# Optimization experiments

Hardware: AMD Instinct MI355X
Metric: run time of the kernel (lower is better)

Reference implementation:

```python
import jax, jax.numpy as jnp
import numpy as np

EPS = 1e-6      # vnn EPS used in norms / leaky-relu denominators
BN_EPS = 1e-5   # torch BatchNorm eps
K = 20          # args.n_knn


def vnlin(W, x):
    # VNLinear: apply (O,C) weight over channel axis 1 of x (B,C,3,...)
    return jnp.moveaxis(jnp.tensordot(W, x, axes=((1,), (1,))), 0, 1)


def vn_bn(x):
    # VNBatchNorm (training-mode batch stats, affine = identity init):
    # normalizes the per-vector norms, rescales vectors accordingly.
    norm = jnp.sqrt(jnp.sum(x * x, axis=2)) + EPS        # (B,C,...)
    axes = (0,) + tuple(range(2, norm.ndim))             # per-channel stats
    mean = jnp.mean(norm, axis=axes, keepdims=True)
    var = jnp.var(norm, axis=axes, keepdims=True)
    norm_bn = (norm - mean) / jnp.sqrt(var + BN_EPS)
    return x / jnp.expand_dims(norm, 2) * jnp.expand_dims(norm_bn, 2)


def vn_lrelu(Wf, Wd, x):
    # VNLinearLeakyReLU with negative_slope=0 (as constructed in this module)
    p = vn_bn(vnlin(Wf, x))
    d = vnlin(Wd, x)
    dot = jnp.sum(p * d, axis=2, keepdims=True)
    dsq = jnp.sum(d * d, axis=2, keepdims=True)
    return jnp.where(dot >= 0, p, p - (dot / (dsq + EPS)) * d)


def vn_maxpool(Wd, x):
    # VNMaxPool: pool over last axis, picking per (b,c) the vector maximizing <x,d>
    d = vnlin(Wd, x)
    dot = jnp.sum(x * d, axis=2, keepdims=True)          # (B,C,1,...)
    idx = jnp.argmax(dot, axis=-1)                       # (B,C,1,...)
    idx = jnp.broadcast_to(idx[..., None], x.shape[:-1] + (1,))
    return jnp.take_along_axis(x, idx, axis=-1)[..., 0]


def graph_feature_cross(x, k):
    # x: (B,3,N) -> (B, 3ch, 3vec, N, k); channels = [nbr-x, x, cross(nbr,x)]
    xx = jnp.sum(x * x, axis=1)                          # (B,N)
    inner = jnp.einsum('bdi,bdj->bij', x, x)             # (B,N,N)
    pd = 2.0 * inner - xx[:, :, None] - xx[:, None, :]   # = -||xi-xj||^2
    idx = jax.lax.top_k(pd, k)[1]                        # (B,N,k) nearest
    pts = jnp.swapaxes(x, 1, 2)                          # (B,N,3)
    nb = jax.vmap(lambda p, i: p[i])(pts, idx)           # (B,N,k,3) gather
    c = jnp.broadcast_to(pts[:, :, None, :], nb.shape)   # center repeated
    cross = jnp.cross(nb, c)
    feat = jnp.stack([nb - c, c, cross], axis=3)         # (B,N,k,3,3)
    return jnp.transpose(feat, (0, 3, 4, 1, 2))


_W_SPECS = {
    'pos_Wf': (21, 3), 'pos_Wd': (21, 3), 'pool_Wd': (21, 21),
    'c1_Wf': (21, 21), 'c1_Wd': (21, 21),
    'st1_Wf': (21, 21), 'st1_Wd': (21, 21),
    'st2_Wf': (42, 21), 'st2_Wd': (42, 21),
    'st3_Wf': (341, 42), 'st3_Wd': (341, 42),
    'st_pool_Wd': (341, 341),
    'stf1_Wf': (170, 341), 'stf1_Wd': (170, 341),
    'stf2_Wf': (85, 170), 'stf2_Wd': (85, 170),
    'stf3_W': (21, 85),
    'c2_Wf': (42, 42), 'c2_Wd': (42, 42),
    'c3_W': (341, 42),
    'std1_Wf': (341, 682), 'std1_Wd': (341, 682),
    'std2_Wf': (170, 341), 'std2_Wd': (170, 341),
    'std_lin': (3, 170),
}


def setup_inputs() -> dict:
    key = jax.random.key(0)
    ks = iter(jax.random.split(key, 32))
    inp = {'x': jax.random.normal(next(ks), (8, 3, 4096), dtype=jnp.float32)}
    for name, (o, i) in _W_SPECS.items():
        inp[name] = jax.random.normal(next(ks), (o, i), dtype=jnp.float32) / np.sqrt(i).astype(np.float32)
    return inp


def _forward(x, pos_Wf, pos_Wd, pool_Wd, c1_Wf, c1_Wd, st1_Wf, st1_Wd, st2_Wf, st2_Wd,
             st3_Wf, st3_Wd, st_pool_Wd, stf1_Wf, stf1_Wd, stf2_Wf, stf2_Wd, stf3_W,
             c2_Wf, c2_Wd, c3_W, std1_Wf, std1_Wd, std2_Wf, std2_Wd, std_lin):
    B, D, N = x.shape
    feat = graph_feature_cross(x, K)                     # (B,3,3,N,k)
    h = vn_lrelu(pos_Wf, pos_Wd, feat)                   # (B,21,3,N,k)
    h = vn_maxpool(pool_Wd, h)                           # (B,21,3,N) pool over k
    h = vn_lrelu(c1_Wf, c1_Wd, h)                        # (B,21,3,N)
    # STNkd feature transform
    s = vn_lrelu(st1_Wf, st1_Wd, h)                      # (B,21,3,N)
    s = vn_lrelu(st2_Wf, st2_Wd, s)                      # (B,42,3,N)
    s = vn_lrelu(st3_Wf, st3_Wd, s)                      # (B,341,3,N)
    s = vn_maxpool(st_pool_Wd, s)                        # (B,341,3) pool over N
    s = vn_lrelu(stf1_Wf, stf1_Wd, s)                    # (B,170,3)
    s = vn_lrelu(stf2_Wf, stf2_Wd, s)                    # (B,85,3)
    s = vnlin(stf3_W, s)                                 # (B,21,3)
    s = jnp.broadcast_to(s[..., None], h.shape)          # repeat over N
    h = jnp.concatenate([h, s], axis=1)                  # (B,42,3,N)
    h = vn_lrelu(c2_Wf, c2_Wd, h)                        # (B,42,3,N)
    h = vn_bn(vnlin(c3_W, h))                            # (B,341,3,N)
    h_mean = jnp.broadcast_to(jnp.mean(h, axis=-1, keepdims=True), h.shape)
    h = jnp.concatenate([h, h_mean], axis=1)             # (B,682,3,N)
    # VNStdFeature (normalize_frame=False)
    z0 = vn_lrelu(std1_Wf, std1_Wd, h)                   # (B,341,3,N)
    z0 = vn_lrelu(std2_Wf, std2_Wd, z0)                  # (B,170,3,N)
    z0 = vnlin(std_lin, z0)                              # (B,3,3,N)
    h_std = jnp.einsum('bijm,bjkm->bikm', h, z0)         # (B,682,3,N)
    out = jnp.max(h_std.reshape(B, -1, N), axis=-1)      # (B,2046)
    return out, z0


def reference(x, pos_Wf, pos_Wd, pool_Wd, c1_Wf, c1_Wd, st1_Wf, st1_Wd, st2_Wf, st2_Wd,
              st3_Wf, st3_Wd, st_pool_Wd, stf1_Wf, stf1_Wd, stf2_Wf, stf2_Wd, stf3_W,
              c2_Wf, c2_Wd, c3_W, std1_Wf, std1_Wd, std2_Wf, std2_Wd, std_lin):
    return _forward(x, pos_Wf, pos_Wd, pool_Wd, c1_Wf, c1_Wd, st1_Wf, st1_Wd, st2_Wf,
                    st2_Wd, st3_Wf, st3_Wd, st_pool_Wd, stf1_Wf, stf1_Wd, stf2_Wf,
                    stf2_Wd, stf3_W, c2_Wf, c2_Wd, c3_W, std1_Wf, std1_Wd, std2_Wf,
                    std2_Wd, std_lin)
```

## Files before the change

kernel.cpp:

```cpp
#include <hip/hip_runtime.h>
#include <cstdint>
#include <cstddef>


typedef unsigned short u16;
using bh8  = __attribute__((ext_vector_type(8))) short;
using f32x4 = __attribute__((ext_vector_type(4))) float;

__device__ __forceinline__ float b2f(u16 v) {
  return __uint_as_float(((unsigned)v) << 16);
}
__device__ __forceinline__ u16 f2b(float f) {
  unsigned u = __float_as_uint(f);
  u += 0x7FFFu + ((u >> 16) & 1u);
  return (u16)(u >> 16);
}

__device__ __forceinline__ float ldg(const float* p, size_t i) { return p[i]; }
__device__ __forceinline__ float ldg(const u16* p, size_t i) { return b2f(p[i]); }
__device__ __forceinline__ void st4(float* p, size_t i, float a, float b, float c, float d) {
  float4 v; v.x = a; v.y = b; v.z = c; v.w = d; *(float4*)(p + i) = v;
}

#define FMA4(A, S, V) { A.x += (S)*(V).x; A.y += (S)*(V).y; A.z += (S)*(V).z; A.w += (S)*(V).w; }

__device__ __forceinline__ unsigned long long packKey(float v, int n) {
  unsigned u = __float_as_uint(v);
  u = (u & 0x80000000u) ? ~u : (u | 0x80000000u);
  return ((unsigned long long)u << 32) | (unsigned long long)(0xFFFFFFFFu - (unsigned)n);
}

#define CSWAP(T) { if (c > T) { unsigned long long tmp = T; T = c; c = tmp; } }
__global__ __launch_bounds__(256) void knn_kernel(const float* __restrict__ x,
                                                  int* __restrict__ idxOut, int N) {
  int b = blockIdx.y;
  int wv = threadIdx.x >> 6, lane = threadIdx.x & 63;
  int i = blockIdx.x * 4 + wv;
  const float* xb = x + (size_t)b * 3 * N;
  float xi0 = xb[i], xi1 = xb[N + i], xi2 = xb[2 * (size_t)N + i];
  float xxi = xi0 * xi0 + xi1 * xi1 + xi2 * xi2;
  unsigned long long t0 = 0, t1 = 0, t2 = 0, t3 = 0, t4 = 0, t5 = 0, t6 = 0, t7 = 0;
  #pragma unroll 8
  for (int s = 0; s < 64; ++s) {
    int j = s * 64 + lane;
    float a0 = xb[j], a1 = xb[N + j], a2 = xb[2 * (size_t)N + j];
    float inner = xi0 * a0 + xi1 * a1 + xi2 * a2;
    float xxj = a0 * a0 + a1 * a1 + a2 * a2;
    float pd = 2.f * inner - xxi - xxj;
    unsigned long long c = packKey(pd, j);
    if (c > t7) { CSWAP(t0) CSWAP(t1) CSWAP(t2) CSWAP(t3) CSWAP(t4) CSWAP(t5) CSWAP(t6) CSWAP(t7) }
  }
  int* row = idxOut + ((size_t)b * N + i) * 20;
  for (int kk = 0; kk < 20; ++kk) {
    unsigned long long k = t0;
    #pragma unroll
    for (int off = 1; off < 64; off <<= 1) {
      unsigned long long o = __shfl_xor(k, off);
      if (o > k) k = o;
    }
    if (lane == 0) row[kk] = (int)(0xFFFFFFFFu - (unsigned)(k & 0xFFFFFFFFull));
    if (k == t0) { t0 = t1; t1 = t2; t2 = t3; t3 = t4; t4 = t5; t5 = t6; t6 = t7; t7 = 0; }
  }
}
#undef CSWAP

__global__ __launch_bounds__(256) void pos_stats(const float* __restrict__ x,
                                                 const int* __restrict__ idx,
                                                 const float* __restrict__ Wf,
                                                 float* __restrict__ statSum,
                                                 float* __restrict__ statSq, int N) {
  __shared__ float wf[64];
  __shared__ float part[4][42];
  int tid = threadIdx.x;
  if (tid < 63) wf[tid] = Wf[tid];
  __syncthreads();
  int b = blockIdx.y;
  int lin = blockIdx.x * 256 + tid;
  int n = lin / 20, kk = lin - n * 20;
  const float* xb = x + (size_t)b * 3 * N;
  int j = idx[((size_t)b * N + n) * 20 + kk];
  float c0 = xb[n], c1 = xb[N + n], c2 = xb[2 * (size_t)N + n];
  float a0 = xb[j], a1 = xb[N + j], a2 = xb[2 * (size_t)N + j];
  float e00 = a0 - c0, e01 = a1 - c1, e02 = a2 - c2;
  float e20 = a1 * c2 - a2 * c1, e21 = a2 * c0 - a0 * c2, e22 = a0 * c1 - a1 * c0;
  int lane = tid & 63, wave = tid >> 6;
  #pragma unroll
  for (int c = 0; c < 21; ++c) {
    float w0 = wf[c * 3], w1 = wf[c * 3 + 1], w2 = wf[c * 3 + 2];
    float p0 = w0 * e00 + w1 * c0 + w2 * e20;
    float p1 = w0 * e01 + w1 * c1 + w2 * e21;
    float p2 = w0 * e02 + w1 * c2 + w2 * e22;
    float nr = sqrtf(p0 * p0 + p1 * p1 + p2 * p2) + 1e-6f;
    float u1 = nr, u2 = nr * nr;
    #pragma unroll
    for (int off = 32; off; off >>= 1) { u1 += __shfl_down(u1, off); u2 += __shfl_down(u2, off); }
    if (lane == 0) { part[wave][c] = u1; part[wave][21 + c] = u2; }
  }
  __syncthreads();
  if (tid < 42) {
    float t = part[0][tid] + part[1][tid] + part[2][tid] + part[3][tid];
    if (tid < 21) atomicAdd(&statSum[tid], t);
    else atomicAdd(&statSq[tid - 21], t);
  }
}

__global__ __launch_bounds__(64) void pos_apply(const float* __restrict__ x,
                                                const int* __restrict__ idx,
                                                const float* __restrict__ Wf,
                                                const float* __restrict__ Wd,
                                                const float* __restrict__ Wpool,
                                                const float* __restrict__ statMean,
                                                const float* __restrict__ statIstd,
                                                float* __restrict__ h0, int N) {
  __shared__ float wpool[441];
  __shared__ float hbuf[64];
  int tid = threadIdx.x;
  for (int l = tid; l < 441; l += 64) wpool[l] = Wpool[l];
  int b = blockIdx.y, n = blockIdx.x;
  bool act = tid < 63;
  int c = act ? tid / 3 : 0;
  int v = act ? tid - c * 3 : 0;
  const float* xb = x + (size_t)b * 3 * N;
  float c0 = xb[n], c1 = xb[N + n], c2 = xb[2 * (size_t)N + n];
  float wf0 = 0, wf1 = 0, wf2 = 0, wd0 = 0, wd1 = 0, wd2 = 0, mn = 0, is = 1.f;
  if (act) {
    wf0 = Wf[c * 3]; wf1 = Wf[c * 3 + 1]; wf2 = Wf[c * 3 + 2];
    wd0 = Wd[c * 3]; wd1 = Wd[c * 3 + 1]; wd2 = Wd[c * 3 + 2];
    mn = statMean[c]; is = statIstd[c];
  }
  __syncthreads();
  float best = -3.4e38f, bh = 0.f;
  const int* idxRow = idx + ((size_t)b * N + n) * 20;
  for (int kk = 0; kk < 20; ++kk) {
    int j = idxRow[kk];
    float a0 = xb[j], a1 = xb[N + j], a2 = xb[2 * (size_t)N + j];
    float av  = (v == 0) ? a0 : ((v == 1) ? a1 : a2);
    float cv  = (v == 0) ? c0 : ((v == 1) ? c1 : c2);
    float a1v = (v == 0) ? a1 : ((v == 1) ? a2 : a0);
    float a2v = (v == 0) ? a2 : ((v == 1) ? a0 : a1);
    float c1v = (v == 0) ? c1 : ((v == 1) ? c2 : c0);
    float c2v = (v == 0) ? c2 : ((v == 1) ? c0 : c1);
    float e0 = av - cv;
    float e1 = cv;
    float e2 = a1v * c2v - a2v * c1v;
    float p = wf0 * e0 + wf1 * e1 + wf2 * e2;
    float d = wd0 * e0 + wd1 * e1 + wd2 * e2;
    int base = c * 3;
    float pp = p * p;
    float n2 = __shfl(pp, base) + __shfl(pp, base + 1) + __shfl(pp, base + 2);
    float nr = sqrtf(n2) + 1e-6f;
    float sc = ((nr - mn) * is) / nr;
    float pb = p * sc;
    float pd2 = pb * d, dd = d * d;
    float dot = __shfl(pd2, base) + __shfl(pd2, base + 1) + __shfl(pd2, base + 2);
    float dsq = __shfl(dd, base) + __shfl(dd, base + 1) + __shfl(dd, base + 2);
    float h = (dot >= 0.f) ? pb : pb - (dot / (dsq + 1e-6f)) * d;
    hbuf[tid] = act ? h : 0.f;
    __syncthreads();
    float d2 = 0.f;
    #pragma unroll 7
    for (int cc = 0; cc < 21; ++cc) d2 += wpool[c * 21 + cc] * hbuf[cc * 3 + v];
    float hd = h * d2;
    float dotp = __shfl(hd, base) + __shfl(hd, base + 1) + __shfl(hd, base + 2);
    if (act && dotp > best) { best = dotp; bh = h; }
    __syncthreads();
  }
  if (act) h0[(((size_t)b * 21 + c) * 3 + v) * N + n] = bh;
}

template<int MODE, int CPT, typename TX, typename TY>
__global__ __launch_bounds__(256) void gemm_vn(
    const float* __restrict__ Wf,
    const TX* __restrict__ X, TY* __restrict__ Y,
    float* __restrict__ statSum, float* __restrict__ statSq,
    const float* __restrict__ statMean, const float* __restrict__ statIstd,
    unsigned long long* __restrict__ poolPart,
    int Cin, int Cout, int wstride, int N) {
  __shared__ float Xs[16][3][64];
  __shared__ float Wfs[16 * CPT][17];
  const int tid = threadIdx.x;
  const int tx = tid & 15, ty = tid >> 4;
  const int b = blockIdx.z;
  const int n0 = blockIdx.x * 64;
  const int co0 = blockIdx.y * (16 * CPT);
  const TX* Xb = X + (size_t)b * Cin * 3 * N;

  float4 acc[CPT][3];
  #pragma unroll
  for (int c = 0; c < CPT; ++c)
    #pragma unroll
    for (int v = 0; v < 3; ++v) acc[c][v] = {0.f, 0.f, 0.f, 0.f};

  for (int k0 = 0; k0 < Cin; k0 += 16) {
    #pragma unroll
    for (int l0 = 0; l0 < 12; ++l0) {
      int l = l0 * 256 + tid;
      int n = l & 63, v = (l >> 6) % 3, kk = l / 192;
      int ci = k0 + kk;
      Xs[kk][v][n] = (ci < Cin) ? ldg(Xb, ((size_t)ci * 3 + v) * N + n0 + n) : 0.f;
    }
    {
      int kk = tid & 15, coL = tid >> 4, ci = k0 + kk;
      #pragma unroll
      for (int c = 0; c < CPT; ++c) {
        int co = co0 + coL + 16 * c;
        bool ok = (co < Cout) && (ci < Cin);
        Wfs[coL + 16 * c][kk] = ok ? Wf[(size_t)co * wstride + ci] : 0.f;
      }
    }
    __syncthreads();
    #pragma unroll
    for (int kk = 0; kk < 16; ++kk) {
      float4 x0 = *(const float4*)&Xs[kk][0][tx * 4];
      float4 x1 = *(const float4*)&Xs[kk][1][tx * 4];
      float4 x2 = *(const float4*)&Xs[kk][2][tx * 4];
      #pragma unroll
      for (int c = 0; c < CPT; ++c) {
        float w = Wfs[ty + 16 * c][kk];
        FMA4(acc[c][0], w, x0); FMA4(acc[c][1], w, x1); FMA4(acc[c][2], w, x2);
      }
    }
    __syncthreads();
  }

  #pragma unroll
  for (int c = 0; c < CPT; ++c) {
    int co = co0 + ty + 16 * c;
    float p_[3][4];
    #pragma unroll
    for (int v = 0; v < 3; ++v) {
      const float* av = (const float*)&acc[c][v];
      p_[v][0] = av[0]; p_[v][1] = av[1]; p_[v][2] = av[2]; p_[v][3] = av[3];
    }
    if constexpr (MODE == 4) {
      unsigned long long key = 0;
      if (co < Cout) {
        size_t xb2 = ((size_t)co * 3) * N + n0 + tx * 4;
        #pragma unroll
        for (int j = 0; j < 4; ++j) {
          float X0 = ldg(Xb, xb2 + j);
          float X1 = ldg(Xb, xb2 + N + j);
          float X2 = ldg(Xb, xb2 + 2 * (size_t)N + j);
          float dot = X0*p_[0][j] + X1*p_[1][j] + X2*p_[2][j];
          unsigned long long k2 = packKey(dot, n0 + tx * 4 + j);
          if (k2 > key) key = k2;
        }
      }
      #pragma unroll
      for (int off = 8; off; off >>= 1) {
        unsigned long long o = __shfl_down(key, off);
        if (o > key) key = o;
      }
      if (tx == 0 && co < Cout) poolPart[((size_t)b * Cout + co) * 64 + blockIdx.x] = key;
    } else if constexpr (MODE == 5) {
      float s1 = 0.f, s2 = 0.f;
      if (co < Cout) {
        size_t yb = ((size_t)b * Cout + co) * 3 * N + n0 + tx * 4;
        #pragma unroll
        for (int j = 0; j < 4; ++j) {
          float nr = sqrtf(p_[0][j]*p_[0][j] + p_[1][j]*p_[1][j] + p_[2][j]*p_[2][j]) + 1e-6f;
          s1 += nr; s2 += nr * nr;
        }
        st4(Y, yb,                 p_[0][0], p_[0][1], p_[0][2], p_[0][3]);
        st4(Y, yb + N,             p_[1][0], p_[1][1], p_[1][2], p_[1][3]);
        st4(Y, yb + 2 * (size_t)N, p_[2][0], p_[2][1], p_[2][2], p_[2][3]);
      }
      #pragma unroll
      for (int off = 8; off; off >>= 1) { s1 += __shfl_down(s1, off); s2 += __shfl_down(s2, off); }
      if (tx == 0 && co < Cout) { atomicAdd(&statSum[co], s1); atomicAdd(&statSq[co], s2); }
    } else if constexpr (MODE == 6) {
      if (co < Cout) {
        float mn = statMean[co], is = statIstd[co];
        size_t yb = ((size_t)b * Cout + co) * 3 * N + n0 + tx * 4;
        float4 P0 = *(const float4*)&Y[yb];
        float4 P1 = *(const float4*)&Y[yb + N];
        float4 P2 = *(const float4*)&Y[yb + 2 * (size_t)N];
        float pr[3][4] = {{P0.x,P0.y,P0.z,P0.w},{P1.x,P1.y,P1.z,P1.w},{P2.x,P2.y,P2.z,P2.w}};
        float o_[3][4];
        #pragma unroll
        for (int j = 0; j < 4; ++j) {
          float q0 = pr[0][j], q1 = pr[1][j], q2 = pr[2][j];
          float e0 = p_[0][j], e1 = p_[1][j], e2 = p_[2][j];
          float nr = sqrtf(q0*q0 + q1*q1 + q2*q2) + 1e-6f;
          float sc = ((nr - mn) * is) / nr;
          q0 *= sc; q1 *= sc; q2 *= sc;
          float dot = q0*e0 + q1*e1 + q2*e2;
          if (dot < 0.f) {
            float dsq = e0*e0 + e1*e1 + e2*e2;
            float t = dot / (dsq + 1e-6f);
            q0 -= t*e0; q1 -= t*e1; q2 -= t*e2;
          }
          o_[0][j] = q0; o_[1][j] = q1; o_[2][j] = q2;
        }
        st4(Y, yb,                 o_[0][0], o_[0][1], o_[0][2], o_[0][3]);
        st4(Y, yb + N,             o_[1][0], o_[1][1], o_[1][2], o_[1][3]);
        st4(Y, yb + 2 * (size_t)N, o_[2][0], o_[2][1], o_[2][2], o_[2][3]);
      }
    }
  }
}

template<int MODE, int NS>
__global__ __launch_bounds__(256) void mfma2(
    const u16* __restrict__ W, const u16* __restrict__ Xt,
    u16* __restrict__ P, float* __restrict__ Zout,
    const float* __restrict__ biasP, const float* __restrict__ biasD,
    float* __restrict__ statSum, float* __restrict__ statSq,
    const float* __restrict__ statMean, const float* __restrict__ statIstd,
    int Cout, int Cpad, int Kpad, int N) {
  const int tid = threadIdx.x, lane = tid & 63, w = tid >> 6;
  const int quad = lane >> 4, l16 = lane & 15;
  const int b = blockIdx.z, n0 = blockIdx.x * 64, co0 = blockIdx.y * 64;
  const int n = n0 + w * 16 + l16;
  const u16* Xb = Xt + (size_t)b * 3 * N * Kpad;
  f32x4 acc[NS][3];
  #pragma unroll
  for (int s = 0; s < NS; ++s)
    #pragma unroll
    for (int v = 0; v < 3; ++v) acc[s][v] = {0.f, 0.f, 0.f, 0.f};

  for (int k0 = 0; k0 < Kpad; k0 += 32) {
    bh8 bx[3];
    #pragma unroll
    for (int v = 0; v < 3; ++v)
      bx[v] = *(const bh8*)(Xb + ((size_t)v * N + n) * Kpad + k0 + quad * 8);
    #pragma unroll
    for (int s = 0; s < NS; ++s) {
      bh8 a = *(const bh8*)(W + (size_t)(co0 + s * 16 + l16) * Kpad + k0 + quad * 8);
      #pragma unroll
      for (int v = 0; v < 3; ++v)
        acc[s][v] = __builtin_amdgcn_mfma_f32_16x16x32_bf16(a, bx[v], acc[s][v], 0, 0, 0);
    }
  }

  u16* Pb = P + (size_t)b * 3 * N * Cpad;
  #pragma unroll
  for (int s = 0; s < NS; ++s) {
    int cb = co0 + s * 16 + quad * 4;
    if constexpr (MODE == 0) {
      #pragma unroll
      for (int r = 0; r < 4; ++r) {
        int co = cb + r;
        if (co < Cout) {
          size_t zb = (((size_t)b * Cout + co) * 3) * N + n;
          Zout[zb] = acc[s][0][r];
          Zout[zb + N] = acc[s][1][r];
          Zout[zb + 2 * (size_t)N] = acc[s][2][r];
        }
      }
    } else if constexpr (MODE == 1) {
      if (cb < Cpad) {
        float q[3][4];
        #pragma unroll
        for (int r = 0; r < 4; ++r) {
          int co = cb + r;
          float b0 = 0, b1 = 0, b2 = 0;
          if (biasP != nullptr && co < Cout) {
            size_t bi = ((size_t)b * Cout + co) * 3;
            b0 = biasP[bi]; b1 = biasP[bi + 1]; b2 = biasP[bi + 2];
          }
          float q0 = acc[s][0][r] + b0, q1 = acc[s][1][r] + b1, q2 = acc[s][2][r] + b2;
          if (co >= Cout) { q0 = 0.f; q1 = 0.f; q2 = 0.f; }
          q[0][r] = q0; q[1][r] = q1; q[2][r] = q2;
          float nr = sqrtf(q0*q0 + q1*q1 + q2*q2) + 1e-6f;
          float s1 = nr, s2 = nr * nr;
          #pragma unroll
          for (int off = 1; off < 16; off <<= 1) { s1 += __shfl_xor(s1, off); s2 += __shfl_xor(s2, off); }
          if (l16 == 0 && co < Cout) { atomicAdd(&statSum[co], s1); atomicAdd(&statSq[co], s2); }
        }
        #pragma unroll
        for (int v = 0; v < 3; ++v) {
          u16 ob[4];
          ob[0] = f2b(q[v][0]); ob[1] = f2b(q[v][1]); ob[2] = f2b(q[v][2]); ob[3] = f2b(q[v][3]);
          *(ushort4*)(Pb + ((size_t)v * N + n) * Cpad + cb) = *(ushort4*)ob;
        }
      }
    } else {
      if (cb < Cpad) {
        u16 pa[3][4];
        #pragma unroll
        for (int v = 0; v < 3; ++v)
          *(ushort4*)pa[v] = *(const ushort4*)(Pb + ((size_t)v * N + n) * Cpad + cb);
        float o[3][4];
        #pragma unroll
        for (int r = 0; r < 4; ++r) {
          int co = cb + r;
          float r0 = 0.f, r1 = 0.f, r2 = 0.f;
          if (co < Cout) {
            float p0 = b2f(pa[0][r]), p1 = b2f(pa[1][r]), p2 = b2f(pa[2][r]);
            float d0 = acc[s][0][r], d1 = acc[s][1][r], d2 = acc[s][2][r];
            if (biasD != nullptr) {
              size_t bi = ((size_t)b * Cout + co) * 3;
              d0 += biasD[bi]; d1 += biasD[bi + 1]; d2 += biasD[bi + 2];
            }
            float mn = statMean[co], is = statIstd[co];
            float nr = sqrtf(p0*p0 + p1*p1 + p2*p2) + 1e-6f;
            float sc = ((nr - mn) * is) / nr;
            float q0 = p0 * sc, q1 = p1 * sc, q2 = p2 * sc;
            float dot = q0*d0 + q1*d1 + q2*d2;
            if (dot < 0.f) {
              float dsq = d0*d0 + d1*d1 + d2*d2;
              float t = dot / (dsq + 1e-6f);
              q0 -= t*d0; q1 -= t*d1; q2 -= t*d2;
            }
            r0 = q0; r1 = q1; r2 = q2;
          }
          o[0][r] = r0; o[1][r] = r1; o[2][r] = r2;
        }
        #pragma unroll
        for (int v = 0; v < 3; ++v) {
          u16 ob[4];
          ob[0] = f2b(o[v][0]); ob[1] = f2b(o[v][1]); ob[2] = f2b(o[v][2]); ob[3] = f2b(o[v][3]);
          *(ushort4*)(Pb + ((size_t)v * N + n) * Cpad + cb) = *(ushort4*)ob;
        }
      }
    }
  }
}

__global__ void w_to_bf16(const float* __restrict__ W, u16* __restrict__ Wp,
                          int Cout, int Cin, int wstride, int CoutPad, int Kpad) {
  int t = blockIdx.x * 256 + threadIdx.x;
  if (t >= CoutPad * Kpad) return;
  int co = t / Kpad, ci = t - co * Kpad;
  Wp[t] = (co < Cout && ci < Cin) ? f2b(W[(size_t)co * wstride + ci]) : (u16)0;
}

__global__ void zero_kernel(float* p, int n) {
  int t = blockIdx.x * 256 + threadIdx.x;
  if (t < n) p[t] = 0.f;
}

__global__ void finalize_kernel(float* __restrict__ sum, float* __restrict__ sq,
                                float* __restrict__ mean, float* __restrict__ istd,
                                int C, float invCount) {
  int c = blockIdx.x * 256 + threadIdx.x;
  if (c < C) {
    float m = sum[c] * invCount;
    float v = sq[c] * invCount - m * m;
    if (v < 0.f) v = 0.f;
    mean[c] = m;
    istd[c] = 1.f / sqrtf(v + 1e-5f);
  }
  if (c < 512) { sum[c] = 0.f; sq[c] = 0.f; }
}

__global__ __launch_bounds__(64) void pool_reduce(const unsigned long long* __restrict__ part,
                                                  const float* __restrict__ s3,
                                                  float* __restrict__ pooled, int N) {
  int co = blockIdx.x, b = blockIdx.y, lane = threadIdx.x;
  unsigned long long key = part[((size_t)b * 341 + co) * 64 + lane];
  #pragma unroll
  for (int off = 32; off; off >>= 1) {
    unsigned long long o = __shfl_down(key, off);
    if (o > key) key = o;
  }
  if (lane == 0) {
    int n = (int)(0xFFFFFFFFu - (unsigned)(key & 0xFFFFFFFFull));
    size_t base = ((size_t)b * 341 + co) * 3;
    pooled[base + 0] = s3[(base + 0) * N + n];
    pooled[base + 1] = s3[(base + 1) * N + n];
    pooled[base + 2] = s3[(base + 2) * N + n];
  }
}

__global__ __launch_bounds__(64) void stf_lrelu(const float* __restrict__ Wf,
                                                const float* __restrict__ Wd,
                                                const float* __restrict__ X,
                                                float* __restrict__ Y, int Cin, int Cout) {
  __shared__ float P[24], D[24], NORM[8], SC[8], DOT[8], DSQ[8], MS[2];
  int co = blockIdx.x, tid = threadIdx.x;
  if (tid < 48) {
    int l = tid < 24 ? tid : tid - 24;
    int b = l / 3, v = l - b * 3;
    const float* W = (tid < 24 ? Wf : Wd) + (size_t)co * Cin;
    const float* xb = X + ((size_t)b * Cin) * 3 + v;
    float acc = 0.f;
    for (int ci = 0; ci < Cin; ++ci) acc += W[ci] * xb[ci * 3];
    if (tid < 24) P[l] = acc; else D[l] = acc;
  }
  __syncthreads();
  if (tid < 8) NORM[tid] = sqrtf(P[tid*3]*P[tid*3] + P[tid*3+1]*P[tid*3+1] + P[tid*3+2]*P[tid*3+2]) + 1e-6f;
  __syncthreads();
  if (tid == 0) {
    float m = 0.f;
    for (int b2 = 0; b2 < 8; ++b2) m += NORM[b2];
    m *= 0.125f;
    float var = 0.f;
    for (int b2 = 0; b2 < 8; ++b2) { float dd = NORM[b2] - m; var += dd * dd; }
    var *= 0.125f;
    MS[0] = m; MS[1] = 1.f / sqrtf(var + 1e-5f);
  }
  __syncthreads();
  if (tid < 8) {
    float sc = ((NORM[tid] - MS[0]) * MS[1]) / NORM[tid];
    float dot = 0.f, dsq = 0.f;
    for (int v = 0; v < 3; ++v) {
      float pb = P[tid*3+v] * sc; float dv = D[tid*3+v];
      dot += pb * dv; dsq += dv * dv;
    }
    SC[tid] = sc; DOT[tid] = dot; DSQ[tid] = dsq;
  }
  __syncthreads();
  if (tid < 24) {
    int b = tid / 3;
    float pb = P[tid] * SC[b];
    float o = (DOT[b] >= 0.f) ? pb : pb - (DOT[b] / (DSQ[b] + 1e-6f)) * D[tid];
    Y[((size_t)b * Cout + co) * 3 + (tid - b * 3)] = o;
  }
}

__global__ void vnlin_small(const float* __restrict__ W, const float* __restrict__ X,
                            float* __restrict__ Y, int Cin, int Cout) {
  int t = blockIdx.x * 256 + threadIdx.x;
  if (t >= 8 * Cout * 3) return;
  int v = t % 3, r = t / 3;
  int co = r % Cout, b = r / Cout;
  float acc = 0.f;
  for (int ci = 0; ci < Cin; ++ci) acc += W[(size_t)co * Cin + ci] * X[((size_t)b * Cin + ci) * 3 + v];
  Y[t] = acc;
}

__global__ __launch_bounds__(256) void concat_tt(const float* __restrict__ h1,
                                                 const float* __restrict__ sfin,
                                                 u16* __restrict__ s2bb, int N) {
  __shared__ u16 tile[64][66];
  int b = blockIdx.z, v = blockIdx.y, n0 = blockIdx.x * 64;
  int tn = threadIdx.x & 63, tc = threadIdx.x >> 6;
  for (int c = tc; c < 64; c += 4) {
    u16 val = 0;
    if (c < 21) val = f2b(h1[(((size_t)b * 21 + c) * 3 + v) * N + n0 + tn]);
    else if (c < 42) val = f2b(sfin[((size_t)b * 21 + (c - 21)) * 3 + v]);
    tile[c][tn] = val;
  }
  __syncthreads();
  u16* dst = s2bb + (((size_t)b * 3 + v) * N + n0) * 64;
  for (int n = tc; n < 64; n += 4)
    dst[(size_t)n * 64 + tn] = tile[tn][n];
}

__global__ __launch_bounds__(384) void bn_apply_mean(u16* __restrict__ H,
    const float* __restrict__ sMean, const float* __restrict__ sIstd,
    float* __restrict__ HmAcc, int N) {
  int c = threadIdx.x;
  if (c >= 341) return;
  int b = blockIdx.y, nt = blockIdx.x;
  float mn = sMean[c], is = sIstd[c];
  float a0 = 0.f, a1 = 0.f, a2 = 0.f;
  size_t base = (size_t)b * 3 * N * 352;
  for (int n = nt * 64; n < nt * 64 + 64; ++n) {
    size_t i0 = base + ((size_t)0 * N + n) * 352 + c;
    size_t i1 = base + ((size_t)1 * N + n) * 352 + c;
    size_t i2 = base + ((size_t)2 * N + n) * 352 + c;
    float p0 = b2f(H[i0]), p1 = b2f(H[i1]), p2 = b2f(H[i2]);
    float nr = sqrtf(p0*p0 + p1*p1 + p2*p2) + 1e-6f;
    float sc = ((nr - mn) * is) / nr;
    p0 *= sc; p1 *= sc; p2 *= sc;
    H[i0] = f2b(p0); H[i1] = f2b(p1); H[i2] = f2b(p2);
    a0 += p0; a1 += p1; a2 += p2;
  }
  size_t hb = ((size_t)b * 341 + c) * 3;
  atomicAdd(&HmAcc[hb], a0); atomicAdd(&HmAcc[hb + 1], a1); atomicAdd(&HmAcc[hb + 2], a2);
}

__global__ void hm_finalize(float* Hm, float invN) {
  int t = blockIdx.x * 256 + threadIdx.x;
  if (t < 8 * 341 * 3) Hm[t] *= invN;
}

__global__ void bias_kernel(const float* __restrict__ Wf, const float* __restrict__ Wd,
                            const float* __restrict__ Hm,
                            float* __restrict__ biasP, float* __restrict__ biasD) {
  int t = blockIdx.x * 256 + threadIdx.x;
  if (t >= 8 * 341 * 3) return;
  int v = t % 3, r = t / 3;
  int co = r % 341, b = r / 341;
  const float* hm = Hm + (size_t)b * 1023 + v;
  float ap = 0.f, ad = 0.f;
  for (int j = 0; j < 341; ++j) {
    float h = hm[j * 3];
    ap += Wf[(size_t)co * 682 + 341 + j] * h;
    ad += Wd[(size_t)co * 682 + 341 + j] * h;
  }
  biasP[t] = ap; biasD[t] = ad;
}

__global__ __launch_bounds__(256) void final_max_part(const u16* __restrict__ H,
    const float* __restrict__ Hm, const float* __restrict__ z0,
    float* __restrict__ part, int N, int NT) {
  __shared__ float red[3][4][64];
  int b = blockIdx.z, nt = blockIdx.y;
  int il = threadIdx.x & 63, nsub = threadIdx.x >> 6;
  int i = blockIdx.x * 64 + il;
  bool valid = i < 682, lo = i < 341;
  float c0 = 0, c1 = 0, c2 = 0;
  if (valid && !lo) {
    size_t hb = ((size_t)b * 341 + (i - 341)) * 3;
    c0 = Hm[hb]; c1 = Hm[hb + 1]; c2 = Hm[hb + 2];
  }
  const float* zb = z0 + (size_t)b * 9 * N;
  const u16* Hb = H + (size_t)b * 3 * N * 352;
  float m0 = -3.4e38f, m1 = -3.4e38f, m2 = -3.4e38f;
  int ii = lo ? i : 0;
  int chunk = N / NT, nBeg = nt * chunk;
  for (int n = nBeg + nsub; n < nBeg + chunk; n += 4) {
    float a0, a1, a2;
    if (lo) {
      a0 = b2f(Hb[((size_t)0 * N + n) * 352 + ii]);
      a1 = b2f(Hb[((size_t)1 * N + n) * 352 + ii]);
      a2 = b2f(Hb[((size_t)2 * N + n) * 352 + ii]);
    } else { a0 = c0; a1 = c1; a2 = c2; }
    float s0 = a0 * zb[n]                + a1 * zb[3 * (size_t)N + n] + a2 * zb[6 * (size_t)N + n];
    float s1 = a0 * zb[N + n]            + a1 * zb[4 * (size_t)N + n] + a2 * zb[7 * (size_t)N + n];
    float s2 = a0 * zb[2 * (size_t)N + n]+ a1 * zb[5 * (size_t)N + n] + a2 * zb[8 * (size_t)N + n];
    m0 = fmaxf(m0, s0); m1 = fmaxf(m1, s1); m2 = fmaxf(m2, s2);
  }
  red[0][nsub][il] = m0; red[1][nsub][il] = m1; red[2][nsub][il] = m2;
  __syncthreads();
  if (nsub == 0 && valid) {
    for (int q = 1; q < 4; ++q) {
      m0 = fmaxf(m0, red[0][q][il]); m1 = fmaxf(m1, red[1][q][il]); m2 = fmaxf(m2, red[2][q][il]);
    }
    size_t pb = ((size_t)b * 682 + i) * 3;
    part[(pb + 0) * NT + nt] = m0;
    part[(pb + 1) * NT + nt] = m1;
    part[(pb + 2) * NT + nt] = m2;
  }
}

__global__ void final_max_reduce(const float* __restrict__ part,
                                 float* __restrict__ out, int NT) {
  int t = blockIdx.x * 256 + threadIdx.x;
  if (t >= 8 * 682 * 3) return;
  const float* p = part + (size_t)t * NT;
  float m = p[0];
  for (int k = 1; k < NT; ++k) m = fmaxf(m, p[k]);
  out[t] = m;
}

extern "C" void kernel_launch(void* const* d_in, const int* in_sizes, int n_in,
                              void* d_out, int out_size, void* d_ws, size_t ws_size,
                              hipStream_t stream) {
  (void)in_sizes; (void)n_in; (void)out_size; (void)ws_size;
  const float* x       = (const float*)d_in[0];
  const float* pos_Wf  = (const float*)d_in[1];
  const float* pos_Wd  = (const float*)d_in[2];
  const float* pool_Wd = (const float*)d_in[3];
  const float* c1_Wf   = (const float*)d_in[4];
  const float* c1_Wd   = (const float*)d_in[5];
  const float* st1_Wf  = (const float*)d_in[6];
  const float* st1_Wd  = (const float*)d_in[7];
  const float* st2_Wf  = (const float*)d_in[8];
  const float* st2_Wd  = (const float*)d_in[9];
  const float* st3_Wf  = (const float*)d_in[10];
  const float* st3_Wd  = (const float*)d_in[11];
  const float* stp_Wd  = (const float*)d_in[12];
  const float* stf1_Wf = (const float*)d_in[13];
  const float* stf1_Wd = (const float*)d_in[14];
  const float* stf2_Wf = (const float*)d_in[15];
  const float* stf2_Wd = (const float*)d_in[16];
  const float* stf3_W  = (const float*)d_in[17];
  const float* c2_Wf   = (const float*)d_in[18];
  const float* c2_Wd   = (const float*)d_in[19];
  const float* c3_W    = (const float*)d_in[20];
  const float* std1_Wf = (const float*)d_in[21];
  const float* std1_Wd = (const float*)d_in[22];
  const float* std2_Wf = (const float*)d_in[23];
  const float* std2_Wd = (const float*)d_in[24];
  const float* stdlin  = (const float*)d_in[25];

  float* outv  = (float*)d_out;
  float* z0out = outv + 8 * 2046;

  const int N = 4096;
  const int NT = 32;
  char* ws = (char*)d_ws;
  size_t off = 0;
  auto alloc = [&](size_t bytes) -> char* {
    char* p = ws + off;
    off += (bytes + 255) & ~(size_t)255;
    return p;
  };
  float* stats = (float*)alloc(2048 * sizeof(float));
  float* sSum = stats, *sSq = stats + 512, *sMean = stats + 1024, *sIstd = stats + 1536;
  int* idx = (int*)alloc((size_t)8 * N * 20 * 4);
  unsigned long long* poolPart = (unsigned long long*)alloc((size_t)8 * 341 * 64 * 8);
  float* fmPart = (float*)alloc((size_t)8 * 682 * 3 * NT * 4);
  float* pooled = (float*)alloc(8 * 341 * 3 * 4);
  float* stf1o  = (float*)alloc(8 * 170 * 3 * 4);
  float* stf2o  = (float*)alloc(8 * 85 * 3 * 4);
  float* sfin   = (float*)alloc(8 * 21 * 3 * 4);
  float* Hm     = (float*)alloc(8 * 1023 * 4);
  float* biasP  = (float*)alloc(8 * 341 * 3 * 4);
  float* biasD  = (float*)alloc(8 * 341 * 3 * 4);
  const size_t E21 = (size_t)8 * 21 * 3 * N, E42 = (size_t)8 * 42 * 3 * N;
  const size_t E341 = (size_t)8 * 341 * 3 * N;
  const size_t T352 = (size_t)8 * 3 * N * 352 * 2;
  const size_t T192 = (size_t)8 * 3 * N * 192 * 2;
  const size_t T64  = (size_t)8 * 3 * N * 64 * 2;
  char* regionA = alloc(T352);
  char* regionB = alloc(E341 * 4);
  float* h0  = (float*)regionA;
  float* h1  = h0 + E21;
  float* s1b = h0 + 2 * E21;
  float* s2b = h0 + 3 * E21;
  float* st3o = (float*)regionB;
  u16* Hbuf  = (u16*)regionB;
  u16* Pstd2 = (u16*)(regionB + T352);
  u16* s2bb  = (u16*)(regionB + T352 + T192);
  u16* h2b   = (u16*)(regionB + T352 + T192 + T64);
  u16* Pstd1 = (u16*)regionA;
  u16* W1fp = (u16*)poolPart;
  u16* W1dp = W1fp + 384 * 352;
  u16* W2fp = W1dp + 384 * 352;
  u16* W2dp = W2fp + 192 * 352;
  u16* Wc3p = W2dp + 192 * 352;
  u16* Wc2f = Wc3p + 384 * 64;
  u16* Wc2d = Wc2f + 64 * 64;
  u16* Wzp  = Wc2d + 64 * 64;

  dim3 blk256(256), blk64(64);
  auto run_lrelu32 = [&](const float* Wf, const float* Wd, const float* X, float* Y,
                         int Cin, int Cout, int wstride, float invCnt) {
    dim3 grid(64, (Cout + 31) / 32, 8);
    gemm_vn<5, 2><<<grid, blk256, 0, stream>>>(Wf, X, Y, sSum, sSq,
                                               nullptr, nullptr, nullptr, Cin, Cout, wstride, N);
    finalize_kernel<<<dim3(2), blk256, 0, stream>>>(sSum, sSq, sMean, sIstd, Cout, invCnt);
    gemm_vn<6, 2><<<grid, blk256, 0, stream>>>(Wd, X, Y, nullptr, nullptr,
                                               sMean, sIstd, nullptr, Cin, Cout, wstride, N);
  };
  const float invBN = 1.f / (8.f * N);
  auto run_mfma = [&](const u16* Wf, const u16* Wd, const u16* X, u16* P,
                      const float* bP, const float* bD,
                      int Cout, int Cpad, int Kpad, int coTiles) {
    dim3 grid(64, coTiles, 8);
    mfma2<1, 4><<<grid, blk256, 0, stream>>>(Wf, X, P, nullptr, bP, nullptr,
                                             sSum, sSq, nullptr, nullptr, Cout, Cpad, Kpad, N);
    finalize_kernel<<<dim3(2), blk256, 0, stream>>>(sSum, sSq, sMean, sIstd, Cout, invBN);
    mfma2<2, 4><<<grid, blk256, 0, stream>>>(Wd, X, P, nullptr, nullptr, bD,
                                             nullptr, nullptr, sMean, sIstd, Cout, Cpad, Kpad, N);
  };

  zero_kernel<<<dim3(4), blk256, 0, stream>>>(stats, 1024);
  knn_kernel<<<dim3(N / 4, 8), blk256, 0, stream>>>(x, idx, N);
  pos_stats<<<dim3(N * 20 / 256, 8), blk256, 0, stream>>>(x, idx, pos_Wf, sSum, sSq, N);
  finalize_kernel<<<dim3(2), blk256, 0, stream>>>(sSum, sSq, sMean, sIstd, 21, 1.f / (8.f * N * 20.f));
  pos_apply<<<dim3(N, 8), blk64, 0, stream>>>(x, idx, pos_Wf, pos_Wd, pool_Wd, sMean, sIstd, h0, N);

  run_lrelu32(c1_Wf, c1_Wd, h0, h1, 21, 21, 21, invBN);
  run_lrelu32(st1_Wf, st1_Wd, h1, s1b, 21, 21, 21, invBN);
  run_lrelu32(st2_Wf, st2_Wd, s1b, s2b, 21, 42, 21, invBN);
  run_lrelu32(st3_Wf, st3_Wd, s2b, st3o, 42, 341, 42, invBN);

  gemm_vn<4, 4><<<dim3(64, 6, 8), blk256, 0, stream>>>(stp_Wd, st3o, (float*)nullptr,
                                                       nullptr, nullptr, nullptr, nullptr,
                                                       poolPart, 341, 341, 341, N);
  pool_reduce<<<dim3(341, 8), blk64, 0, stream>>>(poolPart, st3o, pooled, N);

  w_to_bf16<<<dim3((384 * 352 + 255) / 256), blk256, 0, stream>>>(std1_Wf, W1fp, 341, 341, 682, 384, 352);
  w_to_bf16<<<dim3((384 * 352 + 255) / 256), blk256, 0, stream>>>(std1_Wd, W1dp, 341, 341, 682, 384, 352);
  w_to_bf16<<<dim3((192 * 352 + 255) / 256), blk256, 0, stream>>>(std2_Wf, W2fp, 170, 341, 341, 192, 352);
  w_to_bf16<<<dim3((192 * 352 + 255) / 256), blk256, 0, stream>>>(std2_Wd, W2dp, 170, 341, 341, 192, 352);
  w_to_bf16<<<dim3((384 * 64 + 255) / 256), blk256, 0, stream>>>(c3_W, Wc3p, 341, 42, 42, 384, 64);
  w_to_bf16<<<dim3((64 * 64 + 255) / 256), blk256, 0, stream>>>(c2_Wf, Wc2f, 42, 42, 42, 64, 64);
  w_to_bf16<<<dim3((64 * 64 + 255) / 256), blk256, 0, stream>>>(c2_Wd, Wc2d, 42, 42, 42, 64, 64);
  w_to_bf16<<<dim3((16 * 192 + 255) / 256), blk256, 0, stream>>>(stdlin, Wzp, 3, 170, 170, 16, 192);

  stf_lrelu<<<dim3(170), blk64, 0, stream>>>(stf1_Wf, stf1_Wd, pooled, stf1o, 341, 170);
  stf_lrelu<<<dim3(85),  blk64, 0, stream>>>(stf2_Wf, stf2_Wd, stf1o, stf2o, 170, 85);
  vnlin_small<<<dim3(2), blk256, 0, stream>>>(stf3_W, stf2o, sfin, 85, 21);

  concat_tt<<<dim3(N / 64, 3, 8), blk256, 0, stream>>>(h1, sfin, s2bb, N);
  run_mfma(Wc2f, Wc2d, s2bb, h2b, nullptr, nullptr, 42, 64, 64, 1);

  {
    dim3 grid(64, 6, 8);
    mfma2<1, 4><<<grid, blk256, 0, stream>>>(Wc3p, h2b, Hbuf, nullptr, nullptr, nullptr,
                                             sSum, sSq, nullptr, nullptr, 341, 352, 64, N);
  }
  finalize_kernel<<<dim3(2), blk256, 0, stream>>>(sSum, sSq, sMean, sIstd, 341, invBN);
  zero_kernel<<<dim3(32), blk256, 0, stream>>>(Hm, 8 * 1023);
  bn_apply_mean<<<dim3(64, 8), dim3(384), 0, stream>>>(Hbuf, sMean, sIstd, Hm, N);
  hm_finalize<<<dim3(32), blk256, 0, stream>>>(Hm, 1.f / (float)N);
  bias_kernel<<<dim3(32), blk256, 0, stream>>>(std1_Wf, std1_Wd, Hm, biasP, biasD);

  run_mfma(W1fp, W1dp, Hbuf, Pstd1, biasP, biasD, 341, 352, 352, 6);
  run_mfma(W2fp, W2dp, Pstd1, Pstd2, nullptr, nullptr, 170, 192, 352, 3);

  mfma2<0, 1><<<dim3(64, 1, 8), blk256, 0, stream>>>(Wzp, Pstd2, nullptr, z0out,
                                                     nullptr, nullptr, nullptr, nullptr,
                                                     nullptr, nullptr, 3, 16, 192, N);
  final_max_part<<<dim3(11, NT, 8), blk256, 0, stream>>>(Hbuf, Hm, z0out, fmPart, N, NT);
  final_max_reduce<<<dim3((8 * 682 * 3 + 255) / 256), blk256, 0, stream>>>(fmPart, outv, NT);
}
```

Measured before the change: 2.895 ms.

## Double-buffer VN max-pool GEMM with async global-to-LDS loads and padded layouts

Replaces the MODE 4 path of the generic gemm_vn with a dedicated pool kernel. It pads the st3 output to 352 channels and the pool weight to a 384x352 fp32 buffer, so K tiles need no bounds checks. Global loads go straight into LDS via global_load_lds, and two LDS buffers overlap the next tile's load with compute on the current one. The cost is a per-call weight padding kernel, a larger activation buffer, and reliance on uninitialized padded channels of st3o, which should only meet zero weights.

```diff
diff --git a/kernel.cpp b/kernel.cpp
--- a/kernel.cpp
+++ b/kernel.cpp
@@ -174,8 +174,7 @@
     const TX* __restrict__ X, TY* __restrict__ Y,
     float* __restrict__ statSum, float* __restrict__ statSq,
     const float* __restrict__ statMean, const float* __restrict__ statIstd,
-    unsigned long long* __restrict__ poolPart,
-    int Cin, int Cout, int wstride, int N) {
+    int Cin, int Cout, int CoutStride, int wstride, int N) {
   __shared__ float Xs[16][3][64];
   __shared__ float Wfs[16 * CPT][17];
   const int tid = threadIdx.x;
@@ -232,30 +231,10 @@
       const float* av = (const float*)&acc[c][v];
       p_[v][0] = av[0]; p_[v][1] = av[1]; p_[v][2] = av[2]; p_[v][3] = av[3];
     }
-    if constexpr (MODE == 4) {
-      unsigned long long key = 0;
-      if (co < Cout) {
-        size_t xb2 = ((size_t)co * 3) * N + n0 + tx * 4;
-        #pragma unroll
-        for (int j = 0; j < 4; ++j) {
-          float X0 = ldg(Xb, xb2 + j);
-          float X1 = ldg(Xb, xb2 + N + j);
-          float X2 = ldg(Xb, xb2 + 2 * (size_t)N + j);
-          float dot = X0*p_[0][j] + X1*p_[1][j] + X2*p_[2][j];
-          unsigned long long k2 = packKey(dot, n0 + tx * 4 + j);
-          if (k2 > key) key = k2;
-        }
-      }
-      #pragma unroll
-      for (int off = 8; off; off >>= 1) {
-        unsigned long long o = __shfl_down(key, off);
-        if (o > key) key = o;
-      }
-      if (tx == 0 && co < Cout) poolPart[((size_t)b * Cout + co) * 64 + blockIdx.x] = key;
-    } else if constexpr (MODE == 5) {
+    if constexpr (MODE == 5) {
       float s1 = 0.f, s2 = 0.f;
       if (co < Cout) {
-        size_t yb = ((size_t)b * Cout + co) * 3 * N + n0 + tx * 4;
+        size_t yb = ((size_t)b * CoutStride + co) * 3 * N + n0 + tx * 4;
         #pragma unroll
         for (int j = 0; j < 4; ++j) {
           float nr = sqrtf(p_[0][j]*p_[0][j] + p_[1][j]*p_[1][j] + p_[2][j]*p_[2][j]) + 1e-6f;
@@ -271,7 +250,7 @@
     } else if constexpr (MODE == 6) {
       if (co < Cout) {
         float mn = statMean[co], is = statIstd[co];
-        size_t yb = ((size_t)b * Cout + co) * 3 * N + n0 + tx * 4;
+        size_t yb = ((size_t)b * CoutStride + co) * 3 * N + n0 + tx * 4;
         float4 P0 = *(const float4*)&Y[yb];
         float4 P1 = *(const float4*)&Y[yb + N];
         float4 P2 = *(const float4*)&Y[yb + 2 * (size_t)N];
@@ -297,6 +276,93 @@
         st4(Y, yb + 2 * (size_t)N, o_[2][0], o_[2][1], o_[2][2], o_[2][3]);
       }
     }
+  }
+}
+
+__global__ __launch_bounds__(256) void gemm_pool_db(
+    const float* __restrict__ Wp, const float* __restrict__ Xp,
+    unsigned long long* __restrict__ poolPart, int Cout, int N) {
+  constexpr int KP = 352, CPT = 4;
+  __shared__ float Xs[2][16][3][64];
+  __shared__ float Wfs[2][16 * CPT][16];
+  const int tid = threadIdx.x;
+  const int tx = tid & 15, ty = tid >> 4;
+  const int lane = tid & 63, w = tid >> 6;
+  const int b = blockIdx.z;
+  const int n0 = blockIdx.x * 64;
+  const int co0 = blockIdx.y * (16 * CPT);
+  const float* Xb = Xp + (size_t)b * KP * 3 * N;
+
+  auto stage = [&](int k0, int buf) {
+    #pragma unroll
+    for (int l0 = 0; l0 < 12; ++l0) {
+      int q = l0 * 4 + w;
+      int vv = q % 3, kk = q / 3;
+      const float* g = Xb + ((size_t)(k0 + kk) * 3 + vv) * N + n0 + lane;
+      __builtin_amdgcn_global_load_lds(
+          (const __attribute__((address_space(1))) float*)g,
+          (__attribute__((address_space(3))) float*)&Xs[buf][kk][vv][0], 4, 0, 0);
+    }
+    #pragma unroll
+    for (int c = 0; c < CPT; ++c) {
+      const float* g = Wp + (size_t)(co0 + w * 4 + (lane >> 4) + 16 * c) * KP + k0 + (lane & 15);
+      __builtin_amdgcn_global_load_lds(
+          (const __attribute__((address_space(1))) float*)g,
+          (__attribute__((address_space(3))) float*)&Wfs[buf][w * 4 + 16 * c][0], 4, 0, 0);
+    }
+  };
+
+  float4 acc[CPT][3];
+  #pragma unroll
+  for (int c = 0; c < CPT; ++c)
+    #pragma unroll
+    for (int v = 0; v < 3; ++v) acc[c][v] = {0.f, 0.f, 0.f, 0.f};
+
+  stage(0, 0);
+  __syncthreads();
+  constexpr int KT = KP / 16;
+  for (int kt = 0; kt < KT; ++kt) {
+    int buf = kt & 1;
+    if (kt + 1 < KT) stage((kt + 1) * 16, buf ^ 1);
+    #pragma unroll
+    for (int kk = 0; kk < 16; ++kk) {
+      float4 x0 = *(const float4*)&Xs[buf][kk][0][tx * 4];
+      float4 x1 = *(const float4*)&Xs[buf][kk][1][tx * 4];
+      float4 x2 = *(const float4*)&Xs[buf][kk][2][tx * 4];
+      #pragma unroll
+      for (int c = 0; c < CPT; ++c) {
+        float wv = Wfs[buf][ty + 16 * c][kk];
+        FMA4(acc[c][0], wv, x0); FMA4(acc[c][1], wv, x1); FMA4(acc[c][2], wv, x2);
+      }
+    }
+    __syncthreads();
+  }
+
+  #pragma unroll
+  for (int c = 0; c < CPT; ++c) {
+    int co = co0 + ty + 16 * c;
+    unsigned long long key = 0;
+    if (co < Cout) {
+      const float* av0 = (const float*)&acc[c][0];
+      const float* av1 = (const float*)&acc[c][1];
+      const float* av2 = (const float*)&acc[c][2];
+      size_t xb2 = ((size_t)co * 3) * N + n0 + tx * 4;
+      #pragma unroll
+      for (int j = 0; j < 4; ++j) {
+        float X0 = Xb[xb2 + j];
+        float X1 = Xb[xb2 + N + j];
+        float X2 = Xb[xb2 + 2 * (size_t)N + j];
+        float dot = X0 * av0[j] + X1 * av1[j] + X2 * av2[j];
+        unsigned long long k2 = packKey(dot, n0 + tx * 4 + j);
+        if (k2 > key) key = k2;
+      }
+    }
+    #pragma unroll
+    for (int off = 8; off; off >>= 1) {
+      unsigned long long o = __shfl_down(key, off);
+      if (o > key) key = o;
+    }
+    if (tx == 0 && co < Cout) poolPart[((size_t)b * Cout + co) * 64 + blockIdx.x] = key;
   }
 }
 
@@ -426,6 +492,14 @@
   Wp[t] = (co < Cout && ci < Cin) ? f2b(W[(size_t)co * wstride + ci]) : (u16)0;
 }
 
+__global__ void w_to_f32pad(const float* __restrict__ W, float* __restrict__ Wp,
+                            int Cout, int Cin, int wstride, int CoutPad, int Kpad) {
+  int t = blockIdx.x * 256 + threadIdx.x;
+  if (t >= CoutPad * Kpad) return;
+  int co = t / Kpad, ci = t - co * Kpad;
+  Wp[t] = (co < Cout && ci < Cin) ? W[(size_t)co * wstride + ci] : 0.f;
+}
+
 __global__ void zero_kernel(float* p, int n) {
   int t = blockIdx.x * 256 + threadIdx.x;
   if (t < n) p[t] = 0.f;
@@ -457,10 +531,11 @@
   }
   if (lane == 0) {
     int n = (int)(0xFFFFFFFFu - (unsigned)(key & 0xFFFFFFFFull));
-    size_t base = ((size_t)b * 341 + co) * 3;
-    pooled[base + 0] = s3[(base + 0) * N + n];
-    pooled[base + 1] = s3[(base + 1) * N + n];
-    pooled[base + 2] = s3[(base + 2) * N + n];
+    size_t base = ((size_t)b * 352 + co) * 3;
+    size_t obase = ((size_t)b * 341 + co) * 3;
+    pooled[obase + 0] = s3[(base + 0) * N + n];
+    pooled[obase + 1] = s3[(base + 1) * N + n];
+    pooled[obase + 2] = s3[(base + 2) * N + n];
   }
 }
 
@@ -686,6 +761,7 @@
   int* idx = (int*)alloc((size_t)8 * N * 20 * 4);
   unsigned long long* poolPart = (unsigned long long*)alloc((size_t)8 * 341 * 64 * 8);
   float* fmPart = (float*)alloc((size_t)8 * 682 * 3 * NT * 4);
+  float* Wpoolp = (float*)alloc((size_t)384 * 352 * 4);
   float* pooled = (float*)alloc(8 * 341 * 3 * 4);
   float* stf1o  = (float*)alloc(8 * 170 * 3 * 4);
   float* stf2o  = (float*)alloc(8 * 85 * 3 * 4);
@@ -694,12 +770,12 @@
   float* biasP  = (float*)alloc(8 * 341 * 3 * 4);
   float* biasD  = (float*)alloc(8 * 341 * 3 * 4);
   const size_t E21 = (size_t)8 * 21 * 3 * N, E42 = (size_t)8 * 42 * 3 * N;
-  const size_t E341 = (size_t)8 * 341 * 3 * N;
   const size_t T352 = (size_t)8 * 3 * N * 352 * 2;
   const size_t T192 = (size_t)8 * 3 * N * 192 * 2;
   const size_t T64  = (size_t)8 * 3 * N * 64 * 2;
+  const size_t F352 = (size_t)8 * 352 * 3 * N * 4;
   char* regionA = alloc(T352);
-  char* regionB = alloc(E341 * 4);
+  char* regionB = alloc(F352);
   float* h0  = (float*)regionA;
   float* h1  = h0 + E21;
   float* s1b = h0 + 2 * E21;
@@ -721,13 +797,13 @@
 
   dim3 blk256(256), blk64(64);
   auto run_lrelu32 = [&](const float* Wf, const float* Wd, const float* X, float* Y,
-                         int Cin, int Cout, int wstride, float invCnt) {
+                         int Cin, int Cout, int CoutStride, int wstride, float invCnt) {
     dim3 grid(64, (Cout + 31) / 32, 8);
     gemm_vn<5, 2><<<grid, blk256, 0, stream>>>(Wf, X, Y, sSum, sSq,
-                                               nullptr, nullptr, nullptr, Cin, Cout, wstride, N);
+                                               nullptr, nullptr, Cin, Cout, CoutStride, wstride, N);
     finalize_kernel<<<dim3(2), blk256, 0, stream>>>(sSum, sSq, sMean, sIstd, Cout, invCnt);
     gemm_vn<6, 2><<<grid, blk256, 0, stream>>>(Wd, X, Y, nullptr, nullptr,
-                                               sMean, sIstd, nullptr, Cin, Cout, wstride, N);
+                                               sMean, sIstd, Cin, Cout, CoutStride, wstride, N);
   };
   const float invBN = 1.f / (8.f * N);
   auto run_mfma = [&](const u16* Wf, const u16* Wd, const u16* X, u16* P,
@@ -742,19 +818,18 @@
   };
 
   zero_kernel<<<dim3(4), blk256, 0, stream>>>(stats, 1024);
+  w_to_f32pad<<<dim3((384 * 352 + 255) / 256), blk256, 0, stream>>>(stp_Wd, Wpoolp, 341, 341, 341, 384, 352);
   knn_kernel<<<dim3(N / 4, 8), blk256, 0, stream>>>(x, idx, N);
   pos_stats<<<dim3(N * 20 / 256, 8), blk256, 0, stream>>>(x, idx, pos_Wf, sSum, sSq, N);
   finalize_kernel<<<dim3(2), blk256, 0, stream>>>(sSum, sSq, sMean, sIstd, 21, 1.f / (8.f * N * 20.f));
   pos_apply<<<dim3(N, 8), blk64, 0, stream>>>(x, idx, pos_Wf, pos_Wd, pool_Wd, sMean, sIstd, h0, N);
 
-  run_lrelu32(c1_Wf, c1_Wd, h0, h1, 21, 21, 21, invBN);
-  run_lrelu32(st1_Wf, st1_Wd, h1, s1b, 21, 21, 21, invBN);
-  run_lrelu32(st2_Wf, st2_Wd, s1b, s2b, 21, 42, 21, invBN);
-  run_lrelu32(st3_Wf, st3_Wd, s2b, st3o, 42, 341, 42, invBN);
-
-  gemm_vn<4, 4><<<dim3(64, 6, 8), blk256, 0, stream>>>(stp_Wd, st3o, (float*)nullptr,
-                                                       nullptr, nullptr, nullptr, nullptr,
-                                                       poolPart, 341, 341, 341, N);
+  run_lrelu32(c1_Wf, c1_Wd, h0, h1, 21, 21, 21, 21, invBN);
+  run_lrelu32(st1_Wf, st1_Wd, h1, s1b, 21, 21, 21, 21, invBN);
+  run_lrelu32(st2_Wf, st2_Wd, s1b, s2b, 21, 42, 42, 21, invBN);
+  run_lrelu32(st3_Wf, st3_Wd, s2b, st3o, 42, 341, 352, 42, invBN);
+
+  gemm_pool_db<<<dim3(64, 6, 8), blk256, 0, stream>>>(Wpoolp, st3o, poolPart, 341, N);
   pool_reduce<<<dim3(341, 8), blk64, 0, stream>>>(poolPart, st3o, pooled, N);
 
   w_to_bf16<<<dim3((384 * 352 + 255) / 256), blk256, 0, stream>>>(std1_Wf, W1fp, 341, 341, 682, 384, 352);
```

Result: faster. 2.690 ms (-7.1%).
